# Kernel tuning notes

Hardware: AMD Instinct MI355X
Metric: run time of the kernel (lower is better)

## Reference

```python
import jax, jax.numpy as jnp
import numpy as np

N = 50000      # nodes
E = 800000     # edges (before self-loops)
G = 64         # graphs in batch
IN, HID, OUT, H = 128, 64, 64, 4
NEG_SLOPE = 0.2
BN_EPS = 1e-5


def setup_inputs() -> dict:
    key = jax.random.key(0)
    ks = jax.random.split(key, 16)
    s = 0.1
    return {
        "x": jax.random.normal(ks[0], (N, IN), jnp.float32),
        "edge_index": jax.random.randint(ks[1], (2, E), 0, N, dtype=jnp.int64),
        "batch": jnp.sort(jax.random.randint(ks[2], (N,), 0, G, dtype=jnp.int64)),
        "num_graphs": G,
        "W1": jax.random.normal(ks[3], (IN, H * HID), jnp.float32) * s,
        "att_src1": jax.random.normal(ks[4], (H, HID), jnp.float32) * s,
        "att_dst1": jax.random.normal(ks[5], (H, HID), jnp.float32) * s,
        "b1": jnp.zeros((HID,), jnp.float32),
        "W2": jax.random.normal(ks[6], (HID, H * OUT), jnp.float32) * s,
        "att_src2": jax.random.normal(ks[7], (H, OUT), jnp.float32) * s,
        "att_dst2": jax.random.normal(ks[8], (H, OUT), jnp.float32) * s,
        "b2": jnp.zeros((OUT,), jnp.float32),
        "gate_w1": jax.random.normal(ks[9], (OUT, OUT), jnp.float32) * s,
        "gate_b1": jnp.zeros((OUT,), jnp.float32),
        "bn_gamma": jnp.ones((OUT,), jnp.float32),
        "bn_beta": jnp.zeros((OUT,), jnp.float32),
        "gate_w2": jax.random.normal(ks[10], (OUT, 1), jnp.float32) * s,
        "gate_b2": jnp.zeros((1,), jnp.float32),
        "lin_w": jax.random.normal(ks[11], (OUT, 1), jnp.float32) * s,
        "lin_b": jnp.zeros((1,), jnp.float32),
    }


def segment_softmax(e, seg, num_segments):
    # numerically stable softmax over segments (per-destination / per-graph)
    m = jax.ops.segment_max(e, seg, num_segments=num_segments)
    m = jnp.where(jnp.isfinite(m), m, 0.0)
    ex = jnp.exp(e - m[seg])
    den = jax.ops.segment_sum(ex, seg, num_segments=num_segments)
    return ex / (den[seg] + 1e-16)


def gat_conv(x, src, dst, n, W, a_src, a_dst, b, heads, ch):
    h = (x @ W).reshape(n, heads, ch)                 # [N,H,C]
    asrc = jnp.sum(h * a_src, axis=-1)                # [N,H]
    adst = jnp.sum(h * a_dst, axis=-1)                # [N,H]
    e = jax.nn.leaky_relu(asrc[src] + adst[dst], NEG_SLOPE)   # [E',H]
    alpha = segment_softmax(e, dst, n)                # softmax over incoming edges
    out = jax.ops.segment_sum(h[src] * alpha[:, :, None], dst, num_segments=n)
    return jnp.mean(out, axis=1) + b                  # concat=False -> head mean


def reference(x, edge_index, batch, num_graphs, W1, att_src1, att_dst1, b1,
              W2, att_src2, att_dst2, b2, gate_w1, gate_b1, bn_gamma, bn_beta,
              gate_w2, gate_b2, lin_w, lin_b):
    n = x.shape[0]
    loop = jnp.arange(n, dtype=edge_index.dtype)      # PyG add_self_loops default
    src = jnp.concatenate([edge_index[0], loop])
    dst = jnp.concatenate([edge_index[1], loop])

    out = jax.nn.sigmoid(gat_conv(x, src, dst, n, W1, att_src1, att_dst1, b1, H, HID))
    out = jax.nn.sigmoid(gat_conv(out, src, dst, n, W2, att_src2, att_dst2, b2, H, OUT))

    # GlobalAttention pooling; gate_nn = Linear -> BN(eval, rm=0, rv=1) -> ReLU -> Linear
    g = out @ gate_w1 + gate_b1
    g = (g / jnp.sqrt(1.0 + BN_EPS)) * bn_gamma + bn_beta
    g = jax.nn.relu(g) @ gate_w2 + gate_b2            # [N,1]
    gate = segment_softmax(g, batch, num_graphs)      # per-graph softmax
    pooled = jax.ops.segment_sum(gate * out, batch, num_segments=num_graphs)  # [G,OUT]

    return jax.nn.sigmoid(pooled @ lin_w + lin_b)     # [G,1]
```

## Files before the change

### kernel.cpp

```cpp
#include <hip/hip_runtime.h>


constexpr int NN = 50000;
constexpr int EE = 800000;
constexpr int NG = 64;
constexpr float NEG = 0.2f;
constexpr int MT = NN / 16;
constexpr int SLOTS = 64;
constexpr int CH = 16;
constexpr int GB = (MT + 3) / 4;

constexpr int EB_EDGES = 4096;
constexpr int EBN = (EE + EB_EDGES - 1) / EB_EDGES;
constexpr int NBKT = (NN + 255) / 256;
constexpr int CAP = 48;
constexpr int OVFCAP = 8192;

static_assert(NN % 4 == 0, "aggregate barrier assumes no early-exit waves");

using bf16x8 = __attribute__((ext_vector_type(8))) __bf16;
using f32x4  = __attribute__((ext_vector_type(4))) float;
using f32x2  = __attribute__((ext_vector_type(2))) float;

__device__ __forceinline__ float wred(float v) {
#pragma unroll
  for (int o = 32; o; o >>= 1) v += __shfl_down(v, o);
  return v;
}
__device__ __forceinline__ float sigmoidf(float v) { return 1.f / (1.f + __expf(-v)); }
__device__ __forceinline__ float lrelu(float v) { return fmaxf(v, NEG * v); }
__device__ __forceinline__ unsigned short f2b(float f) {
  union { float f; unsigned u; } v; v.f = f;
  unsigned r = v.u + 0x7fff + ((v.u >> 16) & 1);
  return (unsigned short)(r >> 16);
}
__device__ __forceinline__ float b2f(unsigned short b) {
  union { unsigned u; float f; } v; v.u = ((unsigned)b) << 16;
  return v.f;
}

__global__ void prep_kernel(const float* __restrict__ W1, const float* __restrict__ W2,
                            const float* __restrict__ gw1, const float* __restrict__ gamma,
                            const int* __restrict__ batch,
                            unsigned short* __restrict__ W1b, unsigned short* __restrict__ W2b,
                            unsigned short* __restrict__ Bg, int* __restrict__ goffs,
                            int* __restrict__ ovf_cnt) {
  int b = blockIdx.x;
  if (b < 128) {
    int idx = b * 256 + threadIdx.x;
    int j = idx & 7, lane = (idx >> 3) & 63, rest = idx >> 9;
    int kc = rest & 3, ntile = rest >> 2;
    W1b[idx] = f2b(W1[(kc * 32 + (lane >> 4) * 8 + j) * 256 + ntile * 16 + (lane & 15)]);
    return;
  }
  if (b < 192) {
    int idx = (b - 128) * 256 + threadIdx.x;
    int j = idx & 7, lane = (idx >> 3) & 63, rest = idx >> 9;
    int kc = rest & 1, ntile = rest >> 1;
    W2b[idx] = f2b(W2[(kc * 32 + (lane >> 4) * 8 + j) * 256 + ntile * 16 + (lane & 15)]);
    return;
  }
  if (b < 208) {
    int idx = (b - 192) * 256 + threadIdx.x;
    int j = idx & 7, lane = (idx >> 3) & 63, rest = idx >> 9;
    int kc = rest & 1, nt = rest >> 1;
    int k = kc * 32 + (lane >> 4) * 8 + j;
    int n = nt * 16 + (lane & 15);
    Bg[idx] = f2b(gw1[k * 64 + n] * gamma[n] * rsqrtf(1.f + 1e-5f));
    return;
  }
  if (threadIdx.x == 0) *ovf_cnt = 0;
  int g = threadIdx.x;
  if (g <= NG) {
    int lo = 0, hi = NN;
    while (lo < hi) {
      int mid = (lo + hi) >> 1;
      if (batch[mid] < g) lo = mid + 1; else hi = mid;
    }
    goffs[g] = lo;
  }
}

template <int K, bool A32>
__device__ __forceinline__ void gemm_body(int mt, int lane,
                                          const void* __restrict__ A_raw,
                                          const unsigned short* __restrict__ Bp,
                                          unsigned char* __restrict__ C8,
                                          const float* __restrict__ att_s,
                                          const float* __restrict__ att_d,
                                          float* __restrict__ asrc,
                                          float* __restrict__ adst) {
  constexpr int KC = K / 32;
  int m0 = mt * 16;
  int q = lane >> 4, r = lane & 15;
  f32x4 acc[16] = {};
#pragma unroll
  for (int kc = 0; kc < KC; ++kc) {
    bf16x8 a;
    if constexpr (A32) {
      const float* Arow = (const float*)A_raw + (size_t)(m0 + r) * K + q * 8 + kc * 32;
      float4 f0 = *(const float4*)Arow;
      float4 f1 = *(const float4*)(Arow + 4);
      union { bf16x8 v; unsigned short s[8]; } u;
      u.s[0] = f2b(f0.x); u.s[1] = f2b(f0.y); u.s[2] = f2b(f0.z); u.s[3] = f2b(f0.w);
      u.s[4] = f2b(f1.x); u.s[5] = f2b(f1.y); u.s[6] = f2b(f1.z); u.s[7] = f2b(f1.w);
      a = u.v;
    } else {
      a = *(const bf16x8*)((const unsigned short*)A_raw +
                           (size_t)(m0 + r) * K + q * 8 + kc * 32);
    }
#pragma unroll
    for (int nt = 0; nt < 16; ++nt) {
      bf16x8 b = *(const bf16x8*)&Bp[(((size_t)nt * KC + kc) * 64 + lane) * 8];
      acc[nt] = __builtin_amdgcn_mfma_f32_16x16x32_bf16(a, b, acc[nt], 0, 0, 0);
    }
  }
#pragma unroll
  for (int nt = 0; nt < 16; ++nt) {
    unsigned col = nt * 16 + r;
#pragma unroll
    for (int reg = 0; reg < 4; ++reg) {
      unsigned row = m0 + q * 4 + reg;
      int p = __builtin_amdgcn_cvt_pk_fp8_f32(acc[nt][reg], 0.f, 0, false);
      C8[row * 256u + col] = (unsigned char)(p & 0xff);
    }
  }
  float ps[4][4] = {}, pd[4][4] = {};
#pragma unroll
  for (int head = 0; head < 4; ++head) {
#pragma unroll
    for (int i = 0; i < 4; ++i) {
      float sv = att_s[head * 64 + i * 16 + r];
      float dv = att_d[head * 64 + i * 16 + r];
#pragma unroll
      for (int reg = 0; reg < 4; ++reg) {
        ps[head][reg] += acc[head * 4 + i][reg] * sv;
        pd[head][reg] += acc[head * 4 + i][reg] * dv;
      }
    }
  }
#pragma unroll
  for (int head = 0; head < 4; ++head)
#pragma unroll
    for (int reg = 0; reg < 4; ++reg)
#pragma unroll
      for (int o = 1; o < 16; o <<= 1) {
        ps[head][reg] += __shfl_xor(ps[head][reg], o);
        pd[head][reg] += __shfl_xor(pd[head][reg], o);
      }
  if (r == 0) {
#pragma unroll
    for (int reg = 0; reg < 4; ++reg) {
      int row = m0 + q * 4 + reg;
#pragma unroll
      for (int head = 0; head < 4; ++head) {
        asrc[row * 4 + head] = ps[head][reg];
        adst[row * 4 + head] = pd[head][reg];
      }
    }
  }
}

__global__ void gemm1_build_kernel(const float* __restrict__ x,
                                   const unsigned short* __restrict__ W1b,
                                   unsigned char* __restrict__ C8,
                                   const float* __restrict__ att_s,
                                   const float* __restrict__ att_d,
                                   float* __restrict__ asrc, float* __restrict__ adst,
                                   const int* __restrict__ ei,
                                   unsigned* __restrict__ bins,
                                   int* __restrict__ binCnt,
                                   int* __restrict__ ovf_cnt,
                                   unsigned* __restrict__ ovf) {
  int b = blockIdx.x;
  if (b < GB) {
    int wave = threadIdx.x >> 6, lane = threadIdx.x & 63;
    int mt = b * 4 + wave;
    if (mt >= MT) return;
    gemm_body<128, true>(mt, lane, x, W1b, C8, att_s, att_d, asrc, adst);
    return;
  }
  int hb = b - GB;
  __shared__ int hist[NBKT];
  for (int t = threadIdx.x; t < NBKT; t += 256) hist[t] = 0;
  __syncthreads();
  int e0 = hb * EB_EDGES + threadIdx.x * 16;
#pragma unroll
  for (int k4 = 0; k4 < 4; ++k4) {
    int e = e0 + k4 * 4;
    if (e >= EE) break;
    int4 s4 = *(const int4*)&ei[e];
    int4 d4 = *(const int4*)&ei[EE + e];
    int ss[4] = {s4.x, s4.y, s4.z, s4.w};
    int dd[4] = {d4.x, d4.y, d4.z, d4.w};
#pragma unroll
    for (int u = 0; u < 4; ++u) {
      if (e + u >= EE) break;
      int src = ss[u], dst = dd[u];
      int bkt = dst >> 8;
      int r = atomicAdd(&hist[bkt], 1);
      if (r < CAP) {
        bins[((unsigned)hb * NBKT + bkt) * CAP + r] =
            (unsigned)src | ((unsigned)(dst & 255) << 16);
      } else {
        int o = atomicAdd(ovf_cnt, 1);
        if (o < OVFCAP) ovf[o] = (unsigned)src | ((unsigned)dst << 16);
      }
    }
  }
  __syncthreads();
  for (int t = threadIdx.x; t < NBKT; t += 256) binCnt[hb * NBKT + t] = hist[t];
}

__global__ __launch_bounds__(1024) void csr_build_kernel(
    const unsigned* __restrict__ bins, const int* __restrict__ binCnt,
    const int* __restrict__ ovf_cnt, const unsigned* __restrict__ ovf,
    unsigned short* __restrict__ csr16, int* __restrict__ cnt) {
  int b = blockIdx.x;
  __shared__ int hist[256];
  int t = threadIdx.x;
  int node0 = b << 8;
  if (t < 256) {
    hist[t] = 1;
    int node = node0 + t;
    if (node < NN) csr16[(unsigned)node * SLOTS] = (unsigned short)node;
  }
  __syncthreads();
  int wave = t >> 6, lane = t & 63;
  for (int i = wave; i < EBN; i += 16) {
    int c = binCnt[i * NBKT + b];
    if (c > CAP) c = CAP;
    for (int base = 0; base < c; base += 64) {
      int j = base + lane;
      if (j < c) {
        unsigned p = bins[((unsigned)i * NBKT + b) * CAP + j];
        int dl = p >> 16, src = p & 0xffff;
        int r = atomicAdd(&hist[dl], 1);
        if (r < SLOTS) csr16[(unsigned)(node0 + dl) * SLOTS + r] = (unsigned short)src;
      }
    }
  }
  __syncthreads();
  int oc = *ovf_cnt;
  if (oc > OVFCAP) oc = OVFCAP;
  for (int j = t; j < oc; j += 1024) {
    unsigned p = ovf[j];
    int dst = (int)(p >> 16);
    if ((dst >> 8) == b) {
      int r = atomicAdd(&hist[dst & 255], 1);
      if (r < SLOTS) csr16[(unsigned)dst * SLOTS + r] = (unsigned short)(p & 0xffff);
    }
  }
  __syncthreads();
  if (t < 256) {
    int node = node0 + t;
    if (node < NN) cnt[node] = hist[t];
  }
}

__global__ void aggregate_kernel(const unsigned char* __restrict__ h8,
                                 const float* __restrict__ asrc,
                                 const float* __restrict__ adst,
                                 const int* __restrict__ cnt,
                                 const unsigned short* __restrict__ csr_src,
                                 const float* __restrict__ bias,
                                 unsigned short* __restrict__ outb) {
  int wave = threadIdx.x >> 6, lane = threadIdx.x & 63;
  int node = blockIdx.x * 4 + wave;
  int deg = min(cnt[node], SLOTS);
  int hgrp = lane >> 4;
  int q4 = lane >> 4;
  int r16 = lane & 15;
  int hbase = (r16 >> 2) << 4;
  float adh = adst[node * 4 + hgrp];
  int src_all = csr_src[(unsigned)node * SLOTS + lane];
  float wreg[4];
  float den = 0.f;
#pragma unroll
  for (int i = 0; i < 4; ++i) {
    int slot = i * 16 + r16;
    int s = __shfl(src_all, slot);
    bool valid = slot < deg;
    float xv = asrc[(unsigned)(valid ? s : 0) * 4 + hgrp];
    float w = __expf(lrelu(xv + adh));
    wreg[i] = valid ? w : 0.f;
    den += wreg[i];
  }
#pragma unroll
  for (int o = 1; o < 16; o <<= 1) den += __shfl_xor(den, o);

  const unsigned char* hp = h8 + (unsigned)r16 * 16;
  f32x2 a[8] = {};
#define ACC4(d, wv)                                                         \
  {                                                                         \
    a[0] += __builtin_amdgcn_cvt_pk_f32_fp8((d).x, false) * (wv);           \
    a[1] += __builtin_amdgcn_cvt_pk_f32_fp8((d).x, true) * (wv);            \
    a[2] += __builtin_amdgcn_cvt_pk_f32_fp8((d).y, false) * (wv);           \
    a[3] += __builtin_amdgcn_cvt_pk_f32_fp8((d).y, true) * (wv);            \
    a[4] += __builtin_amdgcn_cvt_pk_f32_fp8((d).z, false) * (wv);           \
    a[5] += __builtin_amdgcn_cvt_pk_f32_fp8((d).z, true) * (wv);            \
    a[6] += __builtin_amdgcn_cvt_pk_f32_fp8((d).w, false) * (wv);           \
    a[7] += __builtin_amdgcn_cvt_pk_f32_fp8((d).w, true) * (wv);            \
  }
  int e = 0;
#pragma unroll
  for (int i = 0; i < 4; ++i) {
    if (e >= deg) break;
    float wcur = wreg[i];
    int bound = min(deg, (i + 1) * 16);
    if (bound - e == 16) {
      int eq = e + q4, wq = hbase + q4;
      int s0 = __shfl(src_all, eq);
      int s1 = __shfl(src_all, eq + 4);
      int s2 = __shfl(src_all, eq + 8);
      int s3 = __shfl(src_all, eq + 12);
      float w0 = __shfl(wcur, wq);
      float w1 = __shfl(wcur, wq + 4);
      float w2 = __shfl(wcur, wq + 8);
      float w3 = __shfl(wcur, wq + 12);
      uint4 d0 = *(const uint4*)(hp + ((unsigned)s0 << 8));
      uint4 d1 = *(const uint4*)(hp + ((unsigned)s1 << 8));
      uint4 d2 = *(const uint4*)(hp + ((unsigned)s2 << 8));
      uint4 d3 = *(const uint4*)(hp + ((unsigned)s3 << 8));
      ACC4(d0, w0); ACC4(d1, w1); ACC4(d2, w2); ACC4(d3, w3);
      e += 16;
    } else {
      for (; e < bound; e += 4) {
        int gg = min(4, bound - e);
        int q4e = min(q4, gg - 1);
        int su = __shfl(src_all, e + q4e);
        float wv = __shfl(wcur, hbase + (e & 15) + q4e);
        if (q4 >= gg) wv = 0.f;
        uint4 d = *(const uint4*)(hp + ((unsigned)su << 8));
        ACC4(d, wv);
      }
    }
  }
#undef ACC4
  float den2 = __shfl(den, (r16 >> 2) << 4);
  float inv = 0.25f / (den2 + 1e-16f);
  __shared__ float red[4][1024];
  float* wb = &red[wave][(unsigned)lane * 16];
  f32x4 v0 = {a[0].x * inv, a[0].y * inv, a[1].x * inv, a[1].y * inv};
  f32x4 v1 = {a[2].x * inv, a[2].y * inv, a[3].x * inv, a[3].y * inv};
  f32x4 v2 = {a[4].x * inv, a[4].y * inv, a[5].x * inv, a[5].y * inv};
  f32x4 v3 = {a[6].x * inv, a[6].y * inv, a[7].x * inv, a[7].y * inv};
  *(f32x4*)(wb + 0) = v0;
  *(f32x4*)(wb + 4) = v1;
  *(f32x4*)(wb + 8) = v2;
  *(f32x4*)(wb + 12) = v3;
  __syncthreads();
  const float* rb = &red[wave][0];
  int vbase = (lane >> 4) * 16 + (lane & 15);
  float s = 0.f;
#pragma unroll
  for (int q = 0; q < 4; ++q)
#pragma unroll
    for (int h = 0; h < 4; ++h)
      s += rb[vbase + q * 256 + h * 64];
  float ov = sigmoidf(s + bias[lane]);
  outb[(size_t)node * 64 + lane] = f2b(ov);
}

__global__ void gemm2_kernel(const unsigned short* __restrict__ out1b,
                             const unsigned short* __restrict__ W2b,
                             unsigned char* __restrict__ C8,
                             const float* __restrict__ att_s,
                             const float* __restrict__ att_d,
                             float* __restrict__ asrc, float* __restrict__ adst) {
  int wave = threadIdx.x >> 6, lane = threadIdx.x & 63;
  int mt = blockIdx.x * 4 + wave;
  if (mt >= MT) return;
  gemm_body<64, false>(mt, lane, out1b, W2b, C8, att_s, att_d, asrc, adst);
}

__global__ void pool_partial_kernel(const int* __restrict__ goffs,
                                    const unsigned short* __restrict__ out2b,
                                    const unsigned short* __restrict__ Bg,
                                    const float* __restrict__ gb1,
                                    const float* __restrict__ gamma,
                                    const float* __restrict__ beta,
                                    const float* __restrict__ gw2,
                                    const float* __restrict__ gb2,
                                    float* __restrict__ part_acc,
                                    float* __restrict__ part_den) {
  int b = blockIdx.x, j = blockIdx.y;
  int beg = goffs[b], end = goffs[b + 1];
  int chunk = (end - beg + CH - 1) / CH;
  int cb = beg + j * chunk;
  int ce = min(end, cb + chunk);
  int lane = threadIdx.x & 63, wave = threadIdx.x >> 6;
  int q = lane >> 4, r = lane & 15;
  const float s = rsqrtf(1.f + 1e-5f);
  float gb2v = gb2[0];
  float accv = 0.f, den = 0.f;
  for (int n0 = cb + wave * 16; n0 < ce; n0 += 64) {
    f32x4 acc[4] = {};
    int row = n0 + r;
    if (row >= NN) row = NN - 1;
    const unsigned short* Arow = out2b + (size_t)row * 64 + q * 8;
#pragma unroll
    for (int kc = 0; kc < 2; ++kc) {
      bf16x8 a = *(const bf16x8*)(Arow + kc * 32);
#pragma unroll
      for (int nt = 0; nt < 4; ++nt) {
        bf16x8 b8 = *(const bf16x8*)&Bg[(((size_t)nt * 2 + kc) * 64 + lane) * 8];
        acc[nt] = __builtin_amdgcn_mfma_f32_16x16x32_bf16(a, b8, acc[nt], 0, 0, 0);
      }
    }
    float sum[4] = {0.f, 0.f, 0.f, 0.f};
#pragma unroll
    for (int nt = 0; nt < 4; ++nt) {
      int col = nt * 16 + r;
      float off = gb1[col] * gamma[col] * s + beta[col];
      float w2 = gw2[col];
#pragma unroll
      for (int reg = 0; reg < 4; ++reg)
        sum[reg] += fmaxf(acc[nt][reg] + off, 0.f) * w2;
    }
#pragma unroll
    for (int reg = 0; reg < 4; ++reg)
#pragma unroll
      for (int o = 1; o < 16; o <<= 1) sum[reg] += __shfl_xor(sum[reg], o);
    float gx[4];
#pragma unroll
    for (int reg = 0; reg < 4; ++reg) {
      int n = n0 + q * 4 + reg;
      gx[reg] = (n < ce) ? __expf(sum[reg] + gb2v) : 0.f;
    }
#pragma unroll
    for (int t = 0; t < 16; ++t) {
      int n = n0 + t;
      if (n >= ce) break;
      float gv = __shfl(gx[t & 3], (t >> 2) << 4);
      accv += gv * b2f(out2b[(size_t)n * 64 + lane]);
      den += gv;
    }
  }
  __shared__ float sacc[4][64];
  __shared__ float sden[4];
  sacc[wave][lane] = accv;
  if (lane == 0) sden[wave] = den;
  __syncthreads();
  if (wave == 0) {
    float a = sacc[0][lane] + sacc[1][lane] + sacc[2][lane] + sacc[3][lane];
    part_acc[((size_t)b * CH + j) * 64 + lane] = a;
    if (lane == 0) part_den[b * CH + j] = sden[0] + sden[1] + sden[2] + sden[3];
  }
}

__global__ void pool_final_kernel(const float* __restrict__ part_acc,
                                  const float* __restrict__ part_den,
                                  const float* __restrict__ lw, const float* __restrict__ lb,
                                  float* __restrict__ out) {
  int b = blockIdx.x, lane = threadIdx.x;
  float a = 0.f;
#pragma unroll
  for (int j = 0; j < CH; ++j) a += part_acc[((size_t)b * CH + j) * 64 + lane];
  float den = (lane < CH) ? part_den[b * CH + lane] : 0.f;
  den = wred(den);
  den = __shfl(den, 0);
  float p = a / (den + 1e-16f);
  float v = wred(p * lw[lane]);
  if (lane == 0) out[b] = sigmoidf(v + lb[0]);
}

extern "C" void kernel_launch(void* const* d_in, const int* in_sizes, int n_in,
                              void* d_out, int out_size, void* d_ws, size_t ws_size,
                              hipStream_t stream) {
  const float* x    = (const float*)d_in[0];
  const int*   ei   = (const int*)d_in[1];
  const int*   batch= (const int*)d_in[2];
  const float* W1   = (const float*)d_in[4];
  const float* as1  = (const float*)d_in[5];
  const float* ad1  = (const float*)d_in[6];
  const float* b1   = (const float*)d_in[7];
  const float* W2   = (const float*)d_in[8];
  const float* as2  = (const float*)d_in[9];
  const float* ad2  = (const float*)d_in[10];
  const float* b2   = (const float*)d_in[11];
  const float* gw1  = (const float*)d_in[12];
  const float* gb1  = (const float*)d_in[13];
  const float* gamma= (const float*)d_in[14];
  const float* beta = (const float*)d_in[15];
  const float* gw2  = (const float*)d_in[16];
  const float* gb2  = (const float*)d_in[17];
  const float* lw   = (const float*)d_in[18];
  const float* lb   = (const float*)d_in[19];
  float* out = (float*)d_out;

  char* ws = (char*)d_ws;
  size_t off = 0;
  auto alloc = [&](size_t bytes) -> void* {
    void* p = ws + off;
    off = (off + bytes + 255) & ~(size_t)255;
    return p;
  };
  unsigned short* W1b    = (unsigned short*)alloc((size_t)128 * 256 * 2);
  unsigned short* W2b    = (unsigned short*)alloc((size_t)64 * 256 * 2);
  unsigned short* Bg     = (unsigned short*)alloc((size_t)64 * 64 * 2);
  unsigned char*  h8     = (unsigned char*)alloc((size_t)NN * 256);
  unsigned short* out1b  = (unsigned short*)alloc((size_t)NN * 64 * 2);
  unsigned short* out2b  = (unsigned short*)alloc((size_t)NN * 64 * 2);
  float*    asrc    = (float*)alloc((size_t)NN * 4 * 4);
  float*    adst    = (float*)alloc((size_t)NN * 4 * 4);
  int*      cnt     = (int*)alloc((size_t)NN * 4);
  unsigned short* csr16 = (unsigned short*)alloc((size_t)NN * SLOTS * 2);
  unsigned* bins    = (unsigned*)alloc((size_t)EBN * NBKT * CAP * 4);
  int*      binCnt  = (int*)alloc((size_t)EBN * NBKT * 4);
  int*      ovf_cnt = (int*)alloc(256);
  unsigned* ovf     = (unsigned*)alloc((size_t)OVFCAP * 4);
  int*      goffs   = (int*)alloc((size_t)(NG + 1) * 4);
  float*    pacc    = (float*)alloc((size_t)NG * CH * 64 * 4);
  float*    pden    = (float*)alloc((size_t)NG * CH * 4);

  const int nodeBlocks = NN / 4;

  prep_kernel<<<209, 256, 0, stream>>>(W1, W2, gw1, gamma, batch,
                                       W1b, W2b, Bg, goffs, ovf_cnt);

  gemm1_build_kernel<<<GB + EBN, 256, 0, stream>>>(x, W1b, h8, as1, ad1, asrc, adst,
                                                   ei, bins, binCnt, ovf_cnt, ovf);
  csr_build_kernel<<<NBKT, 1024, 0, stream>>>(bins, binCnt, ovf_cnt, ovf, csr16, cnt);

  aggregate_kernel<<<nodeBlocks, 256, 0, stream>>>(h8, asrc, adst, cnt, csr16, b1, out1b);

  gemm2_kernel<<<GB, 256, 0, stream>>>(out1b, W2b, h8, as2, ad2, asrc, adst);
  aggregate_kernel<<<nodeBlocks, 256, 0, stream>>>(h8, asrc, adst, cnt, csr16, b2, out2b);

  pool_partial_kernel<<<dim3(NG, CH), 256, 0, stream>>>(goffs, out2b, Bg, gb1, gamma, beta,
                                                        gw2, gb2, pacc, pden);
  pool_final_kernel<<<NG, 64, 0, stream>>>(pacc, pden, lw, lb, out);
}
```

Baseline: 248.8 us.

## Repack fp8 feature layout per channel, stage GEMM weights in LDS

The GEMM epilogue now packs the 16 column tiles of each row into one 16-byte vector store, so each lane writes all head/tile values for its channel in one go. This replaces the old byte-wise fp8 stores with a per-channel interleaved layout. The aggregate kernel is rewritten to match: it applies per-head attention weights to each 4-byte group and pads its LDS reduction buffer to avoid bank conflicts. Both GEMM kernels also copy the weight matrix into shared memory and issue all A-row loads up front, which costs extra LDS and a block barrier.

```diff
diff --git a/kernel.cpp b/kernel.cpp
--- a/kernel.cpp
+++ b/kernel.cpp
@@ -81,49 +81,43 @@
   }
 }
 
-template <int K, bool A32>
-__device__ __forceinline__ void gemm_body(int mt, int lane,
-                                          const void* __restrict__ A_raw,
-                                          const unsigned short* __restrict__ Bp,
+template <int KC>
+__device__ __forceinline__ void gemm_body(int mt, int lane, const bf16x8* av,
+                                          const unsigned short* Bp,
                                           unsigned char* __restrict__ C8,
                                           const float* __restrict__ att_s,
                                           const float* __restrict__ att_d,
                                           float* __restrict__ asrc,
                                           float* __restrict__ adst) {
-  constexpr int KC = K / 32;
   int m0 = mt * 16;
   int q = lane >> 4, r = lane & 15;
   f32x4 acc[16] = {};
 #pragma unroll
   for (int kc = 0; kc < KC; ++kc) {
-    bf16x8 a;
-    if constexpr (A32) {
-      const float* Arow = (const float*)A_raw + (size_t)(m0 + r) * K + q * 8 + kc * 32;
-      float4 f0 = *(const float4*)Arow;
-      float4 f1 = *(const float4*)(Arow + 4);
-      union { bf16x8 v; unsigned short s[8]; } u;
-      u.s[0] = f2b(f0.x); u.s[1] = f2b(f0.y); u.s[2] = f2b(f0.z); u.s[3] = f2b(f0.w);
-      u.s[4] = f2b(f1.x); u.s[5] = f2b(f1.y); u.s[6] = f2b(f1.z); u.s[7] = f2b(f1.w);
-      a = u.v;
-    } else {
-      a = *(const bf16x8*)((const unsigned short*)A_raw +
-                           (size_t)(m0 + r) * K + q * 8 + kc * 32);
-    }
 #pragma unroll
     for (int nt = 0; nt < 16; ++nt) {
-      bf16x8 b = *(const bf16x8*)&Bp[(((size_t)nt * KC + kc) * 64 + lane) * 8];
-      acc[nt] = __builtin_amdgcn_mfma_f32_16x16x32_bf16(a, b, acc[nt], 0, 0, 0);
-    }
-  }
-#pragma unroll
-  for (int nt = 0; nt < 16; ++nt) {
-    unsigned col = nt * 16 + r;
-#pragma unroll
-    for (int reg = 0; reg < 4; ++reg) {
-      unsigned row = m0 + q * 4 + reg;
-      int p = __builtin_amdgcn_cvt_pk_fp8_f32(acc[nt][reg], 0.f, 0, false);
-      C8[row * 256u + col] = (unsigned char)(p & 0xff);
-    }
+      bf16x8 b = *(const bf16x8*)&Bp[(((unsigned)nt * KC + kc) * 64 + lane) * 8];
+      acc[nt] = __builtin_amdgcn_mfma_f32_16x16x32_bf16(av[kc], b, acc[nt], 0, 0, 0);
+    }
+  }
+#pragma unroll
+  for (int reg = 0; reg < 4; ++reg) {
+    unsigned row = m0 + q * 4 + reg;
+    uint4 pk;
+    int w;
+    w = __builtin_amdgcn_cvt_pk_fp8_f32(acc[0][reg], acc[1][reg], 0, false);
+    w = __builtin_amdgcn_cvt_pk_fp8_f32(acc[2][reg], acc[3][reg], w, true);
+    pk.x = (unsigned)w;
+    w = __builtin_amdgcn_cvt_pk_fp8_f32(acc[4][reg], acc[5][reg], 0, false);
+    w = __builtin_amdgcn_cvt_pk_fp8_f32(acc[6][reg], acc[7][reg], w, true);
+    pk.y = (unsigned)w;
+    w = __builtin_amdgcn_cvt_pk_fp8_f32(acc[8][reg], acc[9][reg], 0, false);
+    w = __builtin_amdgcn_cvt_pk_fp8_f32(acc[10][reg], acc[11][reg], w, true);
+    pk.z = (unsigned)w;
+    w = __builtin_amdgcn_cvt_pk_fp8_f32(acc[12][reg], acc[13][reg], 0, false);
+    w = __builtin_amdgcn_cvt_pk_fp8_f32(acc[14][reg], acc[15][reg], w, true);
+    pk.w = (unsigned)w;
+    *(uint4*)(C8 + (size_t)row * 256 + (unsigned)r * 16) = pk;
   }
   float ps[4][4] = {}, pd[4][4] = {};
 #pragma unroll
@@ -172,17 +166,45 @@
                                    int* __restrict__ binCnt,
                                    int* __restrict__ ovf_cnt,
                                    unsigned* __restrict__ ovf) {
+  __shared__ union {
+    unsigned short B[128 * 256];
+    int hist[NBKT];
+  } smem;
   int b = blockIdx.x;
   if (b < GB) {
     int wave = threadIdx.x >> 6, lane = threadIdx.x & 63;
-    int mt = b * 4 + wave;
-    if (mt >= MT) return;
-    gemm_body<128, true>(mt, lane, x, W1b, C8, att_s, att_d, asrc, adst);
+    int mt0 = b * 4 + wave;
+    int mt = min(mt0, MT - 1);
+    int q = lane >> 4, r = lane & 15;
+#pragma unroll
+    for (int it = 0; it < 16; ++it)
+      ((uint4*)smem.B)[it * 256 + threadIdx.x] = ((const uint4*)W1b)[it * 256 + threadIdx.x];
+    bf16x8 av[4];
+    {
+      const float* Arow = x + (size_t)(mt * 16 + r) * 128 + q * 8;
+      float4 f0[4], f1[4];
+#pragma unroll
+      for (int kc = 0; kc < 4; ++kc) {
+        f0[kc] = *(const float4*)(Arow + kc * 32);
+        f1[kc] = *(const float4*)(Arow + kc * 32 + 4);
+      }
+#pragma unroll
+      for (int kc = 0; kc < 4; ++kc) {
+        union { bf16x8 v; unsigned short s[8]; } u;
+        u.s[0] = f2b(f0[kc].x); u.s[1] = f2b(f0[kc].y);
+        u.s[2] = f2b(f0[kc].z); u.s[3] = f2b(f0[kc].w);
+        u.s[4] = f2b(f1[kc].x); u.s[5] = f2b(f1[kc].y);
+        u.s[6] = f2b(f1[kc].z); u.s[7] = f2b(f1[kc].w);
+        av[kc] = u.v;
+      }
+    }
+    __syncthreads();
+    if (mt0 >= MT) return;
+    gemm_body<4>(mt, lane, av, smem.B, C8, att_s, att_d, asrc, adst);
     return;
   }
   int hb = b - GB;
-  __shared__ int hist[NBKT];
-  for (int t = threadIdx.x; t < NBKT; t += 256) hist[t] = 0;
+  for (int t = threadIdx.x; t < NBKT; t += 256) smem.hist[t] = 0;
   __syncthreads();
   int e0 = hb * EB_EDGES + threadIdx.x * 16;
 #pragma unroll
@@ -198,9 +220,9 @@
       if (e + u >= EE) break;
       int src = ss[u], dst = dd[u];
       int bkt = dst >> 8;
-      int r = atomicAdd(&hist[bkt], 1);
-      if (r < CAP) {
-        bins[((unsigned)hb * NBKT + bkt) * CAP + r] =
+      int rr = atomicAdd(&smem.hist[bkt], 1);
+      if (rr < CAP) {
+        bins[((unsigned)hb * NBKT + bkt) * CAP + rr] =
             (unsigned)src | ((unsigned)(dst & 255) << 16);
       } else {
         int o = atomicAdd(ovf_cnt, 1);
@@ -209,7 +231,7 @@
     }
   }
   __syncthreads();
-  for (int t = threadIdx.x; t < NBKT; t += 256) binCnt[hb * NBKT + t] = hist[t];
+  for (int t = threadIdx.x; t < NBKT; t += 256) binCnt[hb * NBKT + t] = smem.hist[t];
 }
 
 __global__ __launch_bounds__(1024) void csr_build_kernel(
@@ -271,7 +293,6 @@
   int hgrp = lane >> 4;
   int q4 = lane >> 4;
   int r16 = lane & 15;
-  int hbase = (r16 >> 2) << 4;
   float adh = adst[node * 4 + hgrp];
   int src_all = csr_src[(unsigned)node * SLOTS + lane];
   float wreg[4];
@@ -291,16 +312,16 @@
 
   const unsigned char* hp = h8 + (unsigned)r16 * 16;
   f32x2 a[8] = {};
-#define ACC4(d, wv)                                                         \
-  {                                                                         \
-    a[0] += __builtin_amdgcn_cvt_pk_f32_fp8((d).x, false) * (wv);           \
-    a[1] += __builtin_amdgcn_cvt_pk_f32_fp8((d).x, true) * (wv);            \
-    a[2] += __builtin_amdgcn_cvt_pk_f32_fp8((d).y, false) * (wv);           \
-    a[3] += __builtin_amdgcn_cvt_pk_f32_fp8((d).y, true) * (wv);            \
-    a[4] += __builtin_amdgcn_cvt_pk_f32_fp8((d).z, false) * (wv);           \
-    a[5] += __builtin_amdgcn_cvt_pk_f32_fp8((d).z, true) * (wv);            \
-    a[6] += __builtin_amdgcn_cvt_pk_f32_fp8((d).w, false) * (wv);           \
-    a[7] += __builtin_amdgcn_cvt_pk_f32_fp8((d).w, true) * (wv);            \
+#define ACC4(d, wA, wB, wC, wD)                                              \
+  {                                                                          \
+    a[0] += __builtin_amdgcn_cvt_pk_f32_fp8((d).x, false) * (wA);            \
+    a[1] += __builtin_amdgcn_cvt_pk_f32_fp8((d).x, true) * (wA);             \
+    a[2] += __builtin_amdgcn_cvt_pk_f32_fp8((d).y, false) * (wB);            \
+    a[3] += __builtin_amdgcn_cvt_pk_f32_fp8((d).y, true) * (wB);             \
+    a[4] += __builtin_amdgcn_cvt_pk_f32_fp8((d).z, false) * (wC);            \
+    a[5] += __builtin_amdgcn_cvt_pk_f32_fp8((d).z, true) * (wC);             \
+    a[6] += __builtin_amdgcn_cvt_pk_f32_fp8((d).w, false) * (wD);            \
+    a[7] += __builtin_amdgcn_cvt_pk_f32_fp8((d).w, true) * (wD);             \
   }
   int e = 0;
 #pragma unroll
@@ -309,55 +330,66 @@
     float wcur = wreg[i];
     int bound = min(deg, (i + 1) * 16);
     if (bound - e == 16) {
-      int eq = e + q4, wq = hbase + q4;
+      int eq = e + q4;
       int s0 = __shfl(src_all, eq);
       int s1 = __shfl(src_all, eq + 4);
       int s2 = __shfl(src_all, eq + 8);
       int s3 = __shfl(src_all, eq + 12);
-      float w0 = __shfl(wcur, wq);
-      float w1 = __shfl(wcur, wq + 4);
-      float w2 = __shfl(wcur, wq + 8);
-      float w3 = __shfl(wcur, wq + 12);
+      float w0h0 = __shfl(wcur, q4),      w0h1 = __shfl(wcur, 16 + q4);
+      float w0h2 = __shfl(wcur, 32 + q4), w0h3 = __shfl(wcur, 48 + q4);
+      float w1h0 = __shfl(wcur, q4 + 4),      w1h1 = __shfl(wcur, 16 + q4 + 4);
+      float w1h2 = __shfl(wcur, 32 + q4 + 4), w1h3 = __shfl(wcur, 48 + q4 + 4);
+      float w2h0 = __shfl(wcur, q4 + 8),      w2h1 = __shfl(wcur, 16 + q4 + 8);
+      float w2h2 = __shfl(wcur, 32 + q4 + 8), w2h3 = __shfl(wcur, 48 + q4 + 8);
+      float w3h0 = __shfl(wcur, q4 + 12),      w3h1 = __shfl(wcur, 16 + q4 + 12);
+      float w3h2 = __shfl(wcur, 32 + q4 + 12), w3h3 = __shfl(wcur, 48 + q4 + 12);
       uint4 d0 = *(const uint4*)(hp + ((unsigned)s0 << 8));
       uint4 d1 = *(const uint4*)(hp + ((unsigned)s1 << 8));
       uint4 d2 = *(const uint4*)(hp + ((unsigned)s2 << 8));
       uint4 d3 = *(const uint4*)(hp + ((unsigned)s3 << 8));
-      ACC4(d0, w0); ACC4(d1, w1); ACC4(d2, w2); ACC4(d3, w3);
+      ACC4(d0, w0h0, w0h1, w0h2, w0h3);
+      ACC4(d1, w1h0, w1h1, w1h2, w1h3);
+      ACC4(d2, w2h0, w2h1, w2h2, w2h3);
+      ACC4(d3, w3h0, w3h1, w3h2, w3h3);
       e += 16;
     } else {
       for (; e < bound; e += 4) {
         int gg = min(4, bound - e);
         int q4e = min(q4, gg - 1);
         int su = __shfl(src_all, e + q4e);
-        float wv = __shfl(wcur, hbase + (e & 15) + q4e);
-        if (q4 >= gg) wv = 0.f;
+        int wl = (e & 15) + q4e;
+        float wa = __shfl(wcur, wl),      wb = __shfl(wcur, 16 + wl);
+        float wc = __shfl(wcur, 32 + wl), wd = __shfl(wcur, 48 + wl);
+        if (q4 >= gg) { wa = 0.f; wb = 0.f; wc = 0.f; wd = 0.f; }
         uint4 d = *(const uint4*)(hp + ((unsigned)su << 8));
-        ACC4(d, wv);
+        ACC4(d, wa, wb, wc, wd);
       }
     }
   }
 #undef ACC4
-  float den2 = __shfl(den, (r16 >> 2) << 4);
-  float inv = 0.25f / (den2 + 1e-16f);
-  __shared__ float red[4][1024];
-  float* wb = &red[wave][(unsigned)lane * 16];
-  f32x4 v0 = {a[0].x * inv, a[0].y * inv, a[1].x * inv, a[1].y * inv};
-  f32x4 v1 = {a[2].x * inv, a[2].y * inv, a[3].x * inv, a[3].y * inv};
-  f32x4 v2 = {a[4].x * inv, a[4].y * inv, a[5].x * inv, a[5].y * inv};
-  f32x4 v3 = {a[6].x * inv, a[6].y * inv, a[7].x * inv, a[7].y * inv};
-  *(f32x4*)(wb + 0) = v0;
-  *(f32x4*)(wb + 4) = v1;
-  *(f32x4*)(wb + 8) = v2;
-  *(f32x4*)(wb + 12) = v3;
+  float dh0 = __shfl(den, 0), dh1 = __shfl(den, 16);
+  float dh2 = __shfl(den, 32), dh3 = __shfl(den, 48);
+  float i0 = 0.25f / (dh0 + 1e-16f), i1 = 0.25f / (dh1 + 1e-16f);
+  float i2 = 0.25f / (dh2 + 1e-16f), i3 = 0.25f / (dh3 + 1e-16f);
+  f32x4 v0 = {a[0].x * i0, a[0].y * i0, a[1].x * i0, a[1].y * i0};
+  f32x4 v1 = {a[2].x * i1, a[2].y * i1, a[3].x * i1, a[3].y * i1};
+  f32x4 v2 = {a[4].x * i2, a[4].y * i2, a[5].x * i2, a[5].y * i2};
+  f32x4 v3 = {a[6].x * i3, a[6].y * i3, a[7].x * i3, a[7].y * i3};
+  __shared__ float red[4][1056];
+  float* wb2 = &red[wave][(unsigned)lane * 16 + (lane & 7) * 4];
+  *(f32x4*)(wb2 + 0) = v0;
+  *(f32x4*)(wb2 + 4) = v1;
+  *(f32x4*)(wb2 + 8) = v2;
+  *(f32x4*)(wb2 + 12) = v3;
   __syncthreads();
   const float* rb = &red[wave][0];
-  int vbase = (lane >> 4) * 16 + (lane & 15);
+  int base = (lane & 15) * 16 + (lane & 7) * 4 + (lane >> 4);
   float s = 0.f;
 #pragma unroll
   for (int q = 0; q < 4; ++q)
 #pragma unroll
     for (int h = 0; h < 4; ++h)
-      s += rb[vbase + q * 256 + h * 64];
+      s += rb[q * 256 + base + 4 * h];
   float ov = sigmoidf(s + bias[lane]);
   outb[(size_t)node * 64 + lane] = f2b(ov);
 }
@@ -368,10 +400,23 @@
                              const float* __restrict__ att_s,
                              const float* __restrict__ att_d,
                              float* __restrict__ asrc, float* __restrict__ adst) {
+  __shared__ unsigned short B2[64 * 256];
   int wave = threadIdx.x >> 6, lane = threadIdx.x & 63;
-  int mt = blockIdx.x * 4 + wave;
-  if (mt >= MT) return;
-  gemm_body<64, false>(mt, lane, out1b, W2b, C8, att_s, att_d, asrc, adst);
+  int mt0 = blockIdx.x * 4 + wave;
+  int mt = min(mt0, MT - 1);
+  int q = lane >> 4, r = lane & 15;
+#pragma unroll
+  for (int it = 0; it < 8; ++it)
+    ((uint4*)B2)[it * 256 + threadIdx.x] = ((const uint4*)W2b)[it * 256 + threadIdx.x];
+  bf16x8 av[2];
+  {
+    const unsigned short* Ar = out1b + (size_t)(mt * 16 + r) * 64 + q * 8;
+    av[0] = *(const bf16x8*)(Ar);
+    av[1] = *(const bf16x8*)(Ar + 32);
+  }
+  __syncthreads();
+  if (mt0 >= MT) return;
+  gemm_body<2>(mt, lane, av, B2, C8, att_s, att_d, asrc, adst);
 }
 
 __global__ void pool_partial_kernel(const int* __restrict__ goffs,
```

New measurement: 252.6 us. About the same (+1.5%).
